# Performance work log

Measured on AMD Instinct MI355X. Metric: run time of the kernel, lower is better.

## Reference

```python
import jax, jax.numpy as jnp
import numpy as np

N_NODES = 10000
N_EDGES = 640000
NODE_DIM = 128
EDGE_DIM = 32
OUT_DIM = 128


def setup_inputs() -> dict:
    key = jax.random.key(0)
    k_h, k_e, k_ef, k_w1, k_w2 = jax.random.split(key, 5)
    h = jax.random.normal(k_h, (N_NODES, NODE_DIM), dtype=jnp.float32)
    edge_index = jax.random.randint(k_e, (2, N_EDGES), 0, N_NODES, dtype=jnp.int64)
    edge_features = jax.random.normal(k_ef, (N_EDGES, EDGE_DIM), dtype=jnp.float32)
    in_dim = 2 * NODE_DIM + EDGE_DIM
    # Kaiming-ish init scale for realism
    W1 = jax.random.normal(k_w1, (in_dim, OUT_DIM), dtype=jnp.float32) / np.sqrt(in_dim)
    b1 = jnp.zeros((OUT_DIM,), dtype=jnp.float32)
    W2 = jax.random.normal(k_w2, (OUT_DIM, OUT_DIM), dtype=jnp.float32) / np.sqrt(OUT_DIM)
    b2 = jnp.zeros((OUT_DIM,), dtype=jnp.float32)
    return {"h": h, "edge_index": edge_index, "edge_features": edge_features,
            "n": N_NODES, "W1": W1, "b1": b1, "W2": W2, "b2": b2}


def reference(h, edge_index, edge_features, n, W1, b1, W2, b2):
    rows, cols = edge_index[0], edge_index[1]
    # gather source/target node features + edge features -> [E, 2*node_dim+edge_dim]
    msg_input = jnp.concatenate([h[rows], h[cols], edge_features], axis=-1)
    hidden = jax.nn.relu(msg_input @ W1 + b1)   # [E, out_dim]
    messages = hidden @ W2 + b2                 # [E, out_dim]
    # scatter-add messages onto destination rows -> [n, out_dim]
    out = jax.ops.segment_sum(messages, rows, num_segments=n)
    return out
```

## Files before the change

### kernel.cpp

```cpp
#include <hip/hip_runtime.h>
#include <hip/hip_bf16.h>


typedef __attribute__((ext_vector_type(8))) short bf16x8;
typedef __attribute__((ext_vector_type(4))) float f32x4;

#define ND 128
#define ED 32

__device__ __forceinline__ short f2bf(float x) {
  unsigned int u = __float_as_uint(x);
  unsigned int r = (u + 0x7FFFu + ((u >> 16) & 1u)) >> 16;
  return (short)r;
}

__device__ __forceinline__ float bf2f(short s) {
  return __uint_as_float(((unsigned int)(unsigned short)s) << 16);
}

__device__ __forceinline__ f32x4 bf8lo(bf16x8 v) {
  f32x4 r;
  #pragma unroll
  for (int j = 0; j < 4; ++j) r[j] = bf2f(v[j]);
  return r;
}
__device__ __forceinline__ f32x4 bf8hi(bf16x8 v) {
  f32x4 r;
  #pragma unroll
  for (int j = 0; j < 4; ++j) r[j] = bf2f(v[4 + j]);
  return r;
}

__device__ __forceinline__ int load_idx(const void* ei, long long i, int is64) {
  return is64 ? (int)((const long long*)ei)[i] : ((const int*)ei)[i];
}

__device__ __forceinline__ int detect64(const void* ei) {
  const unsigned int* u = (const unsigned int*)ei;
  int is64 = 1;
  #pragma unroll
  for (int i = 0; i < 16; ++i)
    if (u[2 * i + 1] != 0u) is64 = 0;
  return is64;
}

__device__ __forceinline__ int swz(int c) {
  int ct = c >> 4, cc = c & 15;
  return (ct >> 2) * 64 + (cc >> 2) * 16 + (ct & 3) * 4 + (cc & 3);
}

__global__ __launch_bounds__(256) void prep_hist_kernel(
    const float* __restrict__ W1, const float* __restrict__ W2,
    const void* __restrict__ ei, int* __restrict__ counts,
    int* __restrict__ rank, short* __restrict__ w12t,
    short* __restrict__ w1eA, short* __restrict__ w2t, int E) {
  int b = blockIdx.x;
  if (b < 128) {
    int t = b * 256 + threadIdx.x;
    if (t < 256 * 128) {
      int np = t >> 7, k = t & 127;
      float v = (np < 128) ? W1[k * 128 + np] : W1[(128 + k) * 128 + (np - 128)];
      w12t[t] = f2bf(v);
    }
    if (t < 128 * 128) {
      int n = t >> 7, k = t & 127;
      w2t[t] = f2bf(W2[k * 128 + n]);
    }
    if (t < 8 * 64 * 8) {
      int ct = t >> 9, lane = (t >> 3) & 63, j = t & 7;
      int li = lane & 15, lg = lane >> 4;
      w1eA[t] = f2bf(W1[(256 + lg * 8 + j) * 128 + ct * 16 + li]);
    }
  } else {
    int e = (b - 128) * 256 + threadIdx.x;
    if (e < E) {
      int is64 = detect64(ei);
      int r = load_idx(ei, e, is64);
      rank[e] = atomicAdd(&counts[r], 1);
    }
  }
}

__global__ __launch_bounds__(1024) void scan_kernel(const int* __restrict__ counts,
                                                    int* __restrict__ row_ptr, int n) {
  __shared__ int wtot[16];
  int tid = threadIdx.x;
  int lane = tid & 63, w = tid >> 6;
  int base_i = tid * 16;
  int c[16];
  int tot = 0;
  #pragma unroll
  for (int j = 0; j < 16; ++j) {
    int i = base_i + j;
    c[j] = (i < n) ? counts[i] : 0;
    tot += c[j];
  }
  int x = tot;
  #pragma unroll
  for (int d = 1; d < 64; d <<= 1) {
    int t = __shfl_up(x, d);
    if (lane >= d) x += t;
  }
  if (lane == 63) wtot[w] = x;
  __syncthreads();
  if (w == 0) {
    int y = (lane < 16) ? wtot[lane] : 0;
    #pragma unroll
    for (int d = 1; d < 16; d <<= 1) {
      int t = __shfl_up(y, d);
      if (lane >= d) y += t;
    }
    if (lane < 16) wtot[lane] = y;
  }
  __syncthreads();
  int waveoff = (w == 0) ? 0 : wtot[w - 1];
  int run = waveoff + x - tot;
  if (tid == 0) row_ptr[0] = 0;
  #pragma unroll
  for (int j = 0; j < 16; ++j) {
    int i = base_i + j;
    if (i < n) {
      run += c[j];
      row_ptr[i + 1] = run;
    }
  }
}

__global__ __launch_bounds__(256, 4) void scatter_sg_kernel(
    const void* __restrict__ ei, const int* __restrict__ row_ptr,
    const int* __restrict__ rank, const float* __restrict__ h,
    const short* __restrict__ w12t, const float* __restrict__ b1,
    int2* __restrict__ ec, float* __restrict__ s2, short* __restrict__ g2,
    int N, int E) {
  int b = blockIdx.x;
  int SGB = (N + 63) >> 6;
  if (b < SGB) {
    int lane = threadIdx.x & 63, w = threadIdx.x >> 6;
    int li = lane & 15, lg = lane >> 4;
    int base = b * 64 + w * 16;
    int rowm = base + li;
    if (rowm >= N) rowm = N - 1;
    float breg[8];
    #pragma unroll
    for (int nt = 0; nt < 8; ++nt) breg[nt] = b1[nt * 16 + li];
    f32x4 acc[16];
    #pragma unroll
    for (int nt = 0; nt < 16; ++nt) acc[nt] = (f32x4){0.f, 0.f, 0.f, 0.f};
    #pragma unroll
    for (int kc = 0; kc < 4; ++kc) {
      f32x4 f0 = *(const f32x4*)(h + (size_t)rowm * ND + kc * 32 + lg * 8);
      f32x4 f1 = *(const f32x4*)(h + (size_t)rowm * ND + kc * 32 + lg * 8 + 4);
      bf16x8 a;
      #pragma unroll
      for (int j = 0; j < 4; ++j) { a[j] = f2bf(f0[j]); a[4 + j] = f2bf(f1[j]); }
      #pragma unroll
      for (int nt = 0; nt < 16; ++nt) {
        bf16x8 bb = *(const bf16x8*)(w12t + (nt * 16 + li) * 128 + kc * 32 + lg * 8);
        acc[nt] = __builtin_amdgcn_mfma_f32_16x16x32_bf16(a, bb, acc[nt], 0, 0, 0);
      }
    }
    #pragma unroll
    for (int nt = 0; nt < 16; ++nt)
      #pragma unroll
      for (int r = 0; r < 4; ++r) {
        int row = base + lg * 4 + r;
        if (row < N) {
          if (nt < 8) {
            s2[(size_t)row * 128 + swz(nt * 16 + li)] = acc[nt][r] + breg[nt];
          } else {
            g2[(size_t)row * 128 + swz((nt - 8) * 16 + li)] = f2bf(acc[nt][r]);
          }
        }
      }
  } else {
    int e = (b - SGB) * 256 + threadIdx.x;
    if (e < E) {
      int is64 = detect64(ei);
      int r = load_idx(ei, e, is64);
      int c = load_idx(ei, (long long)E + e, is64);
      ec[row_ptr[r] + rank[e]] = make_int2(e, c);
    }
  }
}

__global__ __launch_bounds__(128) void layer1_kernel(
    const float* __restrict__ s2, const short* __restrict__ g2,
    const float* __restrict__ ef, const int2* __restrict__ ec,
    const short* __restrict__ w1eA, const int* __restrict__ row_ptr,
    float* __restrict__ hsum) {
  int node = blockIdx.x;
  int lane = threadIdx.x & 63;
  int w = threadIdx.x >> 6;
  int li = lane & 15, lg = lane >> 4;
  int rp = row_ptr[node], rpe = row_ptr[node + 1];
  int deg = rpe - rp;
  __shared__ float red[128];

  f32x4 psum[8];
  #pragma unroll
  for (int ct = 0; ct < 8; ++ct) psum[ct] = (f32x4){0.f, 0.f, 0.f, 0.f};

  if (deg > 0) {
    bf16x8 wa[8];
    #pragma unroll
    for (int ct = 0; ct < 8; ++ct)
      wa[ct] = *(const bf16x8*)(w1eA + ((ct * 64 + lane) * 8));
    f32x4 sreg[8];
    #pragma unroll
    for (int ct = 0; ct < 8; ++ct)
      sreg[ct] = *(const f32x4*)(s2 + (size_t)node * 128 + (ct >> 2) * 64 + lg * 16 + (ct & 3) * 4);

    int ntiles = (deg + 15) >> 4;
    int last = rpe - 1;
    auto ppos = [&](int t) {
      int p = rp + t * 16 + li;
      return p > last ? last : p;
    };

    int2 iA = ec[ppos(w)];
    int2 iB = ec[ppos(w + 2)];
    f32x4 eA0 = *(const f32x4*)(ef + (size_t)iA.x * ED + lg * 8);
    f32x4 eA1 = *(const f32x4*)(ef + (size_t)iA.x * ED + lg * 8 + 4);
    const short* gpA = g2 + (size_t)iA.y * 128;
    bf16x8 gA00 = *(const bf16x8*)(gpA + lg * 16);
    bf16x8 gA01 = *(const bf16x8*)(gpA + lg * 16 + 8);
    bf16x8 gA10 = *(const bf16x8*)(gpA + 64 + lg * 16);
    bf16x8 gA11 = *(const bf16x8*)(gpA + 64 + lg * 16 + 8);

    for (int t = w; t < ntiles; t += 2) {
      int2 iC = ec[ppos(t + 4)];
      f32x4 eB0 = *(const f32x4*)(ef + (size_t)iB.x * ED + lg * 8);
      f32x4 eB1 = *(const f32x4*)(ef + (size_t)iB.x * ED + lg * 8 + 4);
      const short* gpB = g2 + (size_t)iB.y * 128;
      bf16x8 gB00 = *(const bf16x8*)(gpB + lg * 16);
      bf16x8 gB01 = *(const bf16x8*)(gpB + lg * 16 + 8);
      bf16x8 gB10 = *(const bf16x8*)(gpB + 64 + lg * 16);
      bf16x8 gB11 = *(const bf16x8*)(gpB + 64 + lg * 16 + 8);
      bf16x8 bfrag;
      #pragma unroll
      for (int j = 0; j < 4; ++j) { bfrag[j] = f2bf(eA0[j]); bfrag[4 + j] = f2bf(eA1[j]); }
      f32x4 acc[8];
      #pragma unroll
      for (int ct = 0; ct < 8; ++ct)
        acc[ct] = __builtin_amdgcn_mfma_f32_16x16x32_bf16(wa[ct], bfrag,
                                                          (f32x4){0.f, 0.f, 0.f, 0.f}, 0, 0, 0);
      if ((t * 16 + li) < deg) {
        #pragma unroll
        for (int ct = 0; ct < 8; ++ct) {
          bf16x8 gr = (ct < 4) ? ((ct & 2) ? gA01 : gA00) : ((ct & 2) ? gA11 : gA10);
          f32x4 gv = (ct & 1) ? bf8hi(gr) : bf8lo(gr);
          f32x4 v = acc[ct] + sreg[ct] + gv;
          #pragma unroll
          for (int r = 0; r < 4; ++r)
            psum[ct][r] += (v[r] > 0.f ? v[r] : 0.f);
        }
      }
      iA = iB; iB = iC;
      eA0 = eB0; eA1 = eB1;
      gA00 = gB00; gA01 = gB01; gA10 = gB10; gA11 = gB11;
    }
  }

  #pragma unroll
  for (int ct = 0; ct < 8; ++ct)
    #pragma unroll
    for (int r = 0; r < 4; ++r) {
      float v = psum[ct][r];
      v += __shfl_xor(v, 1);
      v += __shfl_xor(v, 2);
      v += __shfl_xor(v, 4);
      v += __shfl_xor(v, 8);
      psum[ct][r] = v;
    }
  if (w == 1 && li == 0) {
    #pragma unroll
    for (int ct = 0; ct < 8; ++ct)
      *(f32x4*)(red + ct * 16 + lg * 4) = psum[ct];
  }
  __syncthreads();
  if (w == 0 && li == 0) {
    #pragma unroll
    for (int ct = 0; ct < 8; ++ct) {
      f32x4 o = psum[ct] + *(const f32x4*)(red + ct * 16 + lg * 4);
      *(f32x4*)(hsum + (size_t)node * 128 + ct * 16 + lg * 4) = o;
    }
  }
}

__global__ __launch_bounds__(256) void out_kernel(const float* __restrict__ hsum,
                                                  const short* __restrict__ w2t,
                                                  const float* __restrict__ b2,
                                                  const int* __restrict__ row_ptr,
                                                  float* __restrict__ out, int N) {
  int lane = threadIdx.x & 63, w = threadIdx.x >> 6;
  int li = lane & 15, lg = lane >> 4;
  int base = blockIdx.x * 64 + w * 16;
  int rowm = base + li;
  if (rowm >= N) rowm = N - 1;
  float breg[8];
  #pragma unroll
  for (int nt = 0; nt < 8; ++nt) breg[nt] = b2[nt * 16 + li];
  f32x4 acc[8];
  #pragma unroll
  for (int nt = 0; nt < 8; ++nt) acc[nt] = (f32x4){0.f, 0.f, 0.f, 0.f};
  #pragma unroll
  for (int kc = 0; kc < 4; ++kc) {
    f32x4 f0 = *(const f32x4*)(hsum + (size_t)rowm * 128 + kc * 32 + lg * 8);
    f32x4 f1 = *(const f32x4*)(hsum + (size_t)rowm * 128 + kc * 32 + lg * 8 + 4);
    bf16x8 a;
    #pragma unroll
    for (int j = 0; j < 4; ++j) { a[j] = f2bf(f0[j]); a[4 + j] = f2bf(f1[j]); }
    #pragma unroll
    for (int nt = 0; nt < 8; ++nt) {
      bf16x8 bb = *(const bf16x8*)(w2t + (nt * 16 + li) * 128 + kc * 32 + lg * 8);
      acc[nt] = __builtin_amdgcn_mfma_f32_16x16x32_bf16(a, bb, acc[nt], 0, 0, 0);
    }
  }
  #pragma unroll
  for (int r = 0; r < 4; ++r) {
    int row = base + lg * 4 + r;
    if (row < N) {
      float dg = (float)(row_ptr[row + 1] - row_ptr[row]);
      #pragma unroll
      for (int nt = 0; nt < 8; ++nt)
        out[(size_t)row * 128 + nt * 16 + li] = acc[nt][r] + dg * breg[nt];
    }
  }
}

extern "C" void kernel_launch(void* const* d_in, const int* in_sizes, int n_in,
                              void* d_out, int out_size, void* d_ws, size_t ws_size,
                              hipStream_t stream) {
  const void*  ei = d_in[1];
  const float* ef = (const float*)d_in[2];
  const float* h  = (const float*)d_in[0];
  const float* W1 = (const float*)d_in[4];
  const float* b1 = (const float*)d_in[5];
  const float* W2 = (const float*)d_in[6];
  const float* b2 = (const float*)d_in[7];
  float* out = (float*)d_out;
  int N = in_sizes[0] / ND;
  int E = in_sizes[2] / ED;

  char* ws = (char*)d_ws;
  size_t off = 0;
  auto alloc = [&](size_t bytes) {
    size_t o = off;
    off = (off + bytes + 255) & ~(size_t)255;
    return o;
  };
  int*   counts  = (int*)(ws + alloc((size_t)N * 4));
  int*   row_ptr = (int*)(ws + alloc((size_t)(N + 1) * 4));
  int*   rank    = (int*)(ws + alloc((size_t)E * 4));
  short* w12t    = (short*)(ws + alloc(256 * 128 * 2));
  short* w1eA    = (short*)(ws + alloc(8 * 64 * 8 * 2));
  short* w2t     = (short*)(ws + alloc(128 * 128 * 2));
  float* s2      = (float*)(ws + alloc((size_t)N * 128 * 4));
  short* g2      = (short*)(ws + alloc((size_t)N * 128 * 2));
  float* hsumb   = (float*)(ws + alloc((size_t)N * 128 * 4));
  int2*  ec      = (int2*)(ws + alloc((size_t)E * 8));

  int SGB = (N + 63) >> 6;
  int SCB = (E + 255) / 256;

  hipMemsetAsync(counts, 0, (size_t)N * 4, stream);
  prep_hist_kernel<<<128 + (E + 255) / 256, 256, 0, stream>>>(
      W1, W2, ei, counts, rank, w12t, w1eA, w2t, E);
  scan_kernel<<<1, 1024, 0, stream>>>(counts, row_ptr, N);
  scatter_sg_kernel<<<SGB + SCB, 256, 0, stream>>>(
      ei, row_ptr, rank, h, w12t, b1, ec, s2, g2, N, E);
  layer1_kernel<<<N, 128, 0, stream>>>(s2, g2, ef, ec, w1eA, row_ptr, hsumb);
  out_kernel<<<(N + 63) / 64, 256, 0, stream>>>(hsumb, w2t, b2, row_ptr, out, N);
}
```

Baseline: 142.0 us.

## Balance layer1 work by edge chunks and split waves by output columns

Replaces per-node blocks in the message kernel with blocks covering fixed edge-count chunks, whose node ranges are found by binary search over row_ptr. The two waves now split output columns instead of edge tiles, which removes the shared-memory reduction and block barrier. Edge loads are batched four tiles at a time in place of the previous rolling prefetch. The int64 detection is computed once into a flag, and the histogram is split into its own kernel, adding a launch.

New measurement: 150.7 us. 1.06x slower.

```diff
diff --git a/kernel.cpp b/kernel.cpp
--- a/kernel.cpp
+++ b/kernel.cpp
@@ -7,6 +7,7 @@
 
 #define ND 128
 #define ED 32
+#define CH 64
 
 __device__ __forceinline__ short f2bf(float x) {
   unsigned int u = __float_as_uint(x);
@@ -35,50 +36,44 @@
   return is64 ? (int)((const long long*)ei)[i] : ((const int*)ei)[i];
 }
 
-__device__ __forceinline__ int detect64(const void* ei) {
-  const unsigned int* u = (const unsigned int*)ei;
-  int is64 = 1;
-  #pragma unroll
-  for (int i = 0; i < 16; ++i)
-    if (u[2 * i + 1] != 0u) is64 = 0;
-  return is64;
-}
-
 __device__ __forceinline__ int swz(int c) {
   int ct = c >> 4, cc = c & 15;
   return (ct >> 2) * 64 + (cc >> 2) * 16 + (ct & 3) * 4 + (cc & 3);
 }
 
-__global__ __launch_bounds__(256) void prep_hist_kernel(
+__global__ __launch_bounds__(256) void prep_kernel(
     const float* __restrict__ W1, const float* __restrict__ W2,
-    const void* __restrict__ ei, int* __restrict__ counts,
-    int* __restrict__ rank, short* __restrict__ w12t,
-    short* __restrict__ w1eA, short* __restrict__ w2t, int E) {
-  int b = blockIdx.x;
-  if (b < 128) {
-    int t = b * 256 + threadIdx.x;
-    if (t < 256 * 128) {
-      int np = t >> 7, k = t & 127;
-      float v = (np < 128) ? W1[k * 128 + np] : W1[(128 + k) * 128 + (np - 128)];
-      w12t[t] = f2bf(v);
-    }
-    if (t < 128 * 128) {
-      int n = t >> 7, k = t & 127;
-      w2t[t] = f2bf(W2[k * 128 + n]);
-    }
-    if (t < 8 * 64 * 8) {
-      int ct = t >> 9, lane = (t >> 3) & 63, j = t & 7;
-      int li = lane & 15, lg = lane >> 4;
-      w1eA[t] = f2bf(W1[(256 + lg * 8 + j) * 128 + ct * 16 + li]);
-    }
-  } else {
-    int e = (b - 128) * 256 + threadIdx.x;
-    if (e < E) {
-      int is64 = detect64(ei);
-      int r = load_idx(ei, e, is64);
-      rank[e] = atomicAdd(&counts[r], 1);
-    }
-  }
+    const unsigned int* __restrict__ ei, short* __restrict__ w12t,
+    short* __restrict__ w1eA, short* __restrict__ w2t, int* __restrict__ flag) {
+  if (blockIdx.x == 0 && threadIdx.x == 0) {
+    int is64 = 1;
+    for (int i = 0; i < 16; ++i)
+      if (ei[2 * i + 1] != 0u) is64 = 0;
+    flag[0] = is64;
+  }
+  int t = blockIdx.x * blockDim.x + threadIdx.x;
+  if (t < 256 * 128) {
+    int np = t >> 7, k = t & 127;
+    float v = (np < 128) ? W1[k * 128 + np] : W1[(128 + k) * 128 + (np - 128)];
+    w12t[t] = f2bf(v);
+  }
+  if (t < 128 * 128) {
+    int n = t >> 7, k = t & 127;
+    w2t[t] = f2bf(W2[k * 128 + n]);
+  }
+  if (t < 8 * 64 * 8) {
+    int ct = t >> 9, lane = (t >> 3) & 63, j = t & 7;
+    int li = lane & 15, lg = lane >> 4;
+    w1eA[t] = f2bf(W1[(256 + lg * 8 + j) * 128 + ct * 16 + li]);
+  }
+}
+
+__global__ void hist_kernel(const void* __restrict__ ei, const int* __restrict__ flag,
+                            int* __restrict__ counts, int* __restrict__ rank, int E) {
+  int e = blockIdx.x * blockDim.x + threadIdx.x;
+  if (e >= E) return;
+  int r = load_idx(ei, e, flag[0]);
+  rank[e] = atomicAdd(&counts[r], 1);
 }
 
 __global__ __launch_bounds__(1024) void scan_kernel(const int* __restrict__ counts,
@@ -127,13 +122,14 @@
 }
 
 __global__ __launch_bounds__(256, 4) void scatter_sg_kernel(
-    const void* __restrict__ ei, const int* __restrict__ row_ptr,
-    const int* __restrict__ rank, const float* __restrict__ h,
-    const short* __restrict__ w12t, const float* __restrict__ b1,
-    int2* __restrict__ ec, float* __restrict__ s2, short* __restrict__ g2,
-    int N, int E) {
+    const void* __restrict__ ei, const int* __restrict__ flag,
+    const int* __restrict__ row_ptr, const int* __restrict__ rank,
+    const float* __restrict__ h, const short* __restrict__ w12t,
+    const float* __restrict__ b1, int2* __restrict__ ec, int2* __restrict__ cb,
+    float* __restrict__ s2, short* __restrict__ g2, int N, int E, int nchunks) {
   int b = blockIdx.x;
   int SGB = (N + 63) >> 6;
+  int SCB = (E + 255) >> 8;
   if (b < SGB) {
     int lane = threadIdx.x & 63, w = threadIdx.x >> 6;
     int li = lane & 15, lg = lane >> 4;
@@ -172,13 +168,24 @@
           }
         }
       }
-  } else {
+  } else if (b < SGB + SCB) {
     int e = (b - SGB) * 256 + threadIdx.x;
     if (e < E) {
-      int is64 = detect64(ei);
-      int r = load_idx(ei, e, is64);
-      int c = load_idx(ei, (long long)E + e, is64);
+      int f = flag[0];
+      int r = load_idx(ei, e, f);
+      int c = load_idx(ei, (long long)E + e, f);
       ec[row_ptr[r] + rank[e]] = make_int2(e, c);
+    }
+  } else {
+    int k = (b - SGB - SCB) * 256 + threadIdx.x;
+    if (k < nchunks) {
+      int t0 = k * CH, t1 = t0 + CH;
+      int lo = 0, hi = N;
+      while (lo < hi) { int mid = (lo + hi) >> 1; if (row_ptr[mid] < t0) lo = mid + 1; else hi = mid; }
+      int na = lo;
+      hi = N;
+      while (lo < hi) { int mid = (lo + hi) >> 1; if (row_ptr[mid] < t1) lo = mid + 1; else hi = mid; }
+      cb[k] = make_int2(na, lo);
     }
   }
 }
@@ -187,102 +194,93 @@
     const float* __restrict__ s2, const short* __restrict__ g2,
     const float* __restrict__ ef, const int2* __restrict__ ec,
     const short* __restrict__ w1eA, const int* __restrict__ row_ptr,
-    float* __restrict__ hsum) {
-  int node = blockIdx.x;
+    const int2* __restrict__ cb, float* __restrict__ hsum) {
+  int2 bounds = cb[blockIdx.x];
+  int na = bounds.x, nb = bounds.y;
+  if (na >= nb) return;
   int lane = threadIdx.x & 63;
   int w = threadIdx.x >> 6;
   int li = lane & 15, lg = lane >> 4;
-  int rp = row_ptr[node], rpe = row_ptr[node + 1];
-  int deg = rpe - rp;
-  __shared__ float red[128];
-
-  f32x4 psum[8];
-  #pragma unroll
-  for (int ct = 0; ct < 8; ++ct) psum[ct] = (f32x4){0.f, 0.f, 0.f, 0.f};
-
-  if (deg > 0) {
-    bf16x8 wa[8];
-    #pragma unroll
-    for (int ct = 0; ct < 8; ++ct)
-      wa[ct] = *(const bf16x8*)(w1eA + ((ct * 64 + lane) * 8));
-    f32x4 sreg[8];
-    #pragma unroll
-    for (int ct = 0; ct < 8; ++ct)
-      sreg[ct] = *(const f32x4*)(s2 + (size_t)node * 128 + (ct >> 2) * 64 + lg * 16 + (ct & 3) * 4);
+
+  bf16x8 wa[4];
+  #pragma unroll
+  for (int nt = 0; nt < 4; ++nt)
+    wa[nt] = *(const bf16x8*)(w1eA + ((w * 4 + nt) * 64 + lane) * 8);
+
+  for (int n = na; n < nb; ++n) {
+    int rp = row_ptr[n], rpe = row_ptr[n + 1];
+    int deg = rpe - rp;
+    f32x4 sreg[4];
+    #pragma unroll
+    for (int nt = 0; nt < 4; ++nt)
+      sreg[nt] = *(const f32x4*)(s2 + (size_t)n * 128 + w * 64 + lg * 16 + nt * 4);
+    f32x4 psum[4];
+    #pragma unroll
+    for (int nt = 0; nt < 4; ++nt) psum[nt] = (f32x4){0.f, 0.f, 0.f, 0.f};
 
     int ntiles = (deg + 15) >> 4;
     int last = rpe - 1;
-    auto ppos = [&](int t) {
-      int p = rp + t * 16 + li;
-      return p > last ? last : p;
-    };
-
-    int2 iA = ec[ppos(w)];
-    int2 iB = ec[ppos(w + 2)];
-    f32x4 eA0 = *(const f32x4*)(ef + (size_t)iA.x * ED + lg * 8);
-    f32x4 eA1 = *(const f32x4*)(ef + (size_t)iA.x * ED + lg * 8 + 4);
-    const short* gpA = g2 + (size_t)iA.y * 128;
-    bf16x8 gA00 = *(const bf16x8*)(gpA + lg * 16);
-    bf16x8 gA01 = *(const bf16x8*)(gpA + lg * 16 + 8);
-    bf16x8 gA10 = *(const bf16x8*)(gpA + 64 + lg * 16);
-    bf16x8 gA11 = *(const bf16x8*)(gpA + 64 + lg * 16 + 8);
-
-    for (int t = w; t < ntiles; t += 2) {
-      int2 iC = ec[ppos(t + 4)];
-      f32x4 eB0 = *(const f32x4*)(ef + (size_t)iB.x * ED + lg * 8);
-      f32x4 eB1 = *(const f32x4*)(ef + (size_t)iB.x * ED + lg * 8 + 4);
-      const short* gpB = g2 + (size_t)iB.y * 128;
-      bf16x8 gB00 = *(const bf16x8*)(gpB + lg * 16);
-      bf16x8 gB01 = *(const bf16x8*)(gpB + lg * 16 + 8);
-      bf16x8 gB10 = *(const bf16x8*)(gpB + 64 + lg * 16);
-      bf16x8 gB11 = *(const bf16x8*)(gpB + 64 + lg * 16 + 8);
-      bf16x8 bfrag;
-      #pragma unroll
-      for (int j = 0; j < 4; ++j) { bfrag[j] = f2bf(eA0[j]); bfrag[4 + j] = f2bf(eA1[j]); }
-      f32x4 acc[8];
-      #pragma unroll
-      for (int ct = 0; ct < 8; ++ct)
-        acc[ct] = __builtin_amdgcn_mfma_f32_16x16x32_bf16(wa[ct], bfrag,
-                                                          (f32x4){0.f, 0.f, 0.f, 0.f}, 0, 0, 0);
-      if ((t * 16 + li) < deg) {
-        #pragma unroll
-        for (int ct = 0; ct < 8; ++ct) {
-          bf16x8 gr = (ct < 4) ? ((ct & 2) ? gA01 : gA00) : ((ct & 2) ? gA11 : gA10);
-          f32x4 gv = (ct & 1) ? bf8hi(gr) : bf8lo(gr);
-          f32x4 v = acc[ct] + sreg[ct] + gv;
+    for (int tb = 0; tb < ntiles; tb += 4) {
+      int nact = ntiles - tb;
+      if (nact > 4) nact = 4;
+      int2 ev[4];
+      #pragma unroll
+      for (int m = 0; m < 4; ++m) {
+        int p = rp + (tb + m) * 16 + li;
+        ev[m] = ec[p > last ? last : p];
+      }
+      f32x4 ea[4], eb[4];
+      #pragma unroll
+      for (int m = 0; m < 4; ++m) {
+        const float* ep = ef + (size_t)ev[m].x * ED + lg * 8;
+        ea[m] = *(const f32x4*)ep;
+        eb[m] = *(const f32x4*)(ep + 4);
+      }
+      #pragma unroll
+      for (int m = 0; m < 4; ++m) {
+        if (m < nact) {
+          const short* gp = g2 + (size_t)ev[m].y * 128 + w * 64 + lg * 16;
+          bf16x8 g0 = *(const bf16x8*)gp;
+          bf16x8 g1 = *(const bf16x8*)(gp + 8);
+          bf16x8 bfrag;
           #pragma unroll
-          for (int r = 0; r < 4; ++r)
-            psum[ct][r] += (v[r] > 0.f ? v[r] : 0.f);
+          for (int j = 0; j < 4; ++j) { bfrag[j] = f2bf(ea[m][j]); bfrag[4 + j] = f2bf(eb[m][j]); }
+          f32x4 a0 = __builtin_amdgcn_mfma_f32_16x16x32_bf16(wa[0], bfrag, (f32x4){0.f,0.f,0.f,0.f}, 0, 0, 0);
+          f32x4 a1 = __builtin_amdgcn_mfma_f32_16x16x32_bf16(wa[1], bfrag, (f32x4){0.f,0.f,0.f,0.f}, 0, 0, 0);
+          f32x4 a2 = __builtin_amdgcn_mfma_f32_16x16x32_bf16(wa[2], bfrag, (f32x4){0.f,0.f,0.f,0.f}, 0, 0, 0);
+          f32x4 a3 = __builtin_amdgcn_mfma_f32_16x16x32_bf16(wa[3], bfrag, (f32x4){0.f,0.f,0.f,0.f}, 0, 0, 0);
+          if ((tb + m) * 16 + li < deg) {
+            f32x4 v0 = a0 + sreg[0] + bf8lo(g0);
+            f32x4 v1 = a1 + sreg[1] + bf8hi(g0);
+            f32x4 v2 = a2 + sreg[2] + bf8lo(g1);
+            f32x4 v3 = a3 + sreg[3] + bf8hi(g1);
+            #pragma unroll
+            for (int r = 0; r < 4; ++r) {
+              psum[0][r] += (v0[r] > 0.f ? v0[r] : 0.f);
+              psum[1][r] += (v1[r] > 0.f ? v1[r] : 0.f);
+              psum[2][r] += (v2[r] > 0.f ? v2[r] : 0.f);
+              psum[3][r] += (v3[r] > 0.f ? v3[r] : 0.f);
+            }
+          }
         }
       }
-      iA = iB; iB = iC;
-      eA0 = eB0; eA1 = eB1;
-      gA00 = gB00; gA01 = gB01; gA10 = gB10; gA11 = gB11;
-    }
-  }
-
-  #pragma unroll
-  for (int ct = 0; ct < 8; ++ct)
-    #pragma unroll
-    for (int r = 0; r < 4; ++r) {
-      float v = psum[ct][r];
-      v += __shfl_xor(v, 1);
-      v += __shfl_xor(v, 2);
-      v += __shfl_xor(v, 4);
-      v += __shfl_xor(v, 8);
-      psum[ct][r] = v;
-    }
-  if (w == 1 && li == 0) {
-    #pragma unroll
-    for (int ct = 0; ct < 8; ++ct)
-      *(f32x4*)(red + ct * 16 + lg * 4) = psum[ct];
-  }
-  __syncthreads();
-  if (w == 0 && li == 0) {
-    #pragma unroll
-    for (int ct = 0; ct < 8; ++ct) {
-      f32x4 o = psum[ct] + *(const f32x4*)(red + ct * 16 + lg * 4);
-      *(f32x4*)(hsum + (size_t)node * 128 + ct * 16 + lg * 4) = o;
+    }
+
+    #pragma unroll
+    for (int nt = 0; nt < 4; ++nt)
+      #pragma unroll
+      for (int r = 0; r < 4; ++r) {
+        float v = psum[nt][r];
+        v += __shfl_xor(v, 1);
+        v += __shfl_xor(v, 2);
+        v += __shfl_xor(v, 4);
+        v += __shfl_xor(v, 8);
+        psum[nt][r] = v;
+      }
+    if (li == 0) {
+      #pragma unroll
+      for (int nt = 0; nt < 4; ++nt)
+        *(f32x4*)(hsum + (size_t)n * 128 + w * 64 + nt * 16 + lg * 4) = psum[nt];
     }
   }
 }
@@ -331,9 +329,9 @@
 extern "C" void kernel_launch(void* const* d_in, const int* in_sizes, int n_in,
                               void* d_out, int out_size, void* d_ws, size_t ws_size,
                               hipStream_t stream) {
+  const float* h  = (const float*)d_in[0];
   const void*  ei = d_in[1];
   const float* ef = (const float*)d_in[2];
-  const float* h  = (const float*)d_in[0];
   const float* W1 = (const float*)d_in[4];
   const float* b1 = (const float*)d_in[5];
   const float* W2 = (const float*)d_in[6];
@@ -341,6 +339,7 @@
   float* out = (float*)d_out;
   int N = in_sizes[0] / ND;
   int E = in_sizes[2] / ED;
+  int nchunks = (E + CH - 1) / CH;
 
   char* ws = (char*)d_ws;
   size_t off = 0;
@@ -349,6 +348,7 @@
     off = (off + bytes + 255) & ~(size_t)255;
     return o;
   };
+  int*   flag    = (int*)(ws + alloc(4));
   int*   counts  = (int*)(ws + alloc((size_t)N * 4));
   int*   row_ptr = (int*)(ws + alloc((size_t)(N + 1) * 4));
   int*   rank    = (int*)(ws + alloc((size_t)E * 4));
@@ -359,16 +359,18 @@
   short* g2      = (short*)(ws + alloc((size_t)N * 128 * 2));
   float* hsumb   = (float*)(ws + alloc((size_t)N * 128 * 4));
   int2*  ec      = (int2*)(ws + alloc((size_t)E * 8));
+  int2*  cbb     = (int2*)(ws + alloc((size_t)nchunks * 8));
 
   int SGB = (N + 63) >> 6;
-  int SCB = (E + 255) / 256;
+  int SCB = (E + 255) >> 8;
+  int CBB = (nchunks + 255) >> 8;
 
   hipMemsetAsync(counts, 0, (size_t)N * 4, stream);
-  prep_hist_kernel<<<128 + (E + 255) / 256, 256, 0, stream>>>(
-      W1, W2, ei, counts, rank, w12t, w1eA, w2t, E);
+  prep_kernel<<<128, 256, 0, stream>>>(W1, W2, (const unsigned int*)ei, w12t, w1eA, w2t, flag);
+  hist_kernel<<<(E + 255) / 256, 256, 0, stream>>>(ei, flag, counts, rank, E);
   scan_kernel<<<1, 1024, 0, stream>>>(counts, row_ptr, N);
-  scatter_sg_kernel<<<SGB + SCB, 256, 0, stream>>>(
-      ei, row_ptr, rank, h, w12t, b1, ec, s2, g2, N, E);
-  layer1_kernel<<<N, 128, 0, stream>>>(s2, g2, ef, ec, w1eA, row_ptr, hsumb);
+  scatter_sg_kernel<<<SGB + SCB + CBB, 256, 0, stream>>>(
+      ei, flag, row_ptr, rank, h, w12t, b1, ec, cbb, s2, g2, N, E, nchunks);
+  layer1_kernel<<<nchunks, 128, 0, stream>>>(s2, g2, ef, ec, w1eA, row_ptr, cbb, hsumb);
   out_kernel<<<(N + 63) / 64, 256, 0, stream>>>(hsumb, w2t, b2, row_ptr, out, N);
 }
```

## Replace CSR sort-based aggregation with edge-parallel atomic scatter into hidden sums

Applied to the files above, without the earlier changes.

Drops the scan and the scatter-to-CSR passes, along with the per-node segmented layer-1 kernel. A grid-stride edge kernel now computes relu(hidden) for each 16-edge tile, stages it in LDS, and atomically adds it into a zeroed fp32 hsum buffer. Row and column indices are packed into one 32-bit word with 16 bits each, and the source projection s2 is stored as bf16. This trades sorting and launch overhead for 82M fp32 atomics, which may contend heavily. The 16-bit packing also limits node count to 65536.

Result: slower. 337.6 us (+137.7%).

```diff
diff --git a/kernel.cpp b/kernel.cpp
--- a/kernel.cpp
+++ b/kernel.cpp
@@ -7,6 +7,7 @@
 
 #define ND 128
 #define ED 32
+#define LROW 132
 
 __device__ __forceinline__ short f2bf(float x) {
   unsigned int u = __float_as_uint(x);
@@ -31,19 +32,6 @@
   return r;
 }
 
-__device__ __forceinline__ int load_idx(const void* ei, long long i, int is64) {
-  return is64 ? (int)((const long long*)ei)[i] : ((const int*)ei)[i];
-}
-
-__device__ __forceinline__ int detect64(const void* ei) {
-  const unsigned int* u = (const unsigned int*)ei;
-  int is64 = 1;
-  #pragma unroll
-  for (int i = 0; i < 16; ++i)
-    if (u[2 * i + 1] != 0u) is64 = 0;
-  return is64;
-}
-
 __device__ __forceinline__ int swz(int c) {
   int ct = c >> 4, cc = c & 15;
   return (ct >> 2) * 64 + (cc >> 2) * 16 + (ct & 3) * 4 + (cc & 3);
@@ -52,7 +40,7 @@
 __global__ __launch_bounds__(256) void prep_hist_kernel(
     const float* __restrict__ W1, const float* __restrict__ W2,
     const void* __restrict__ ei, int* __restrict__ counts,
-    int* __restrict__ rank, short* __restrict__ w12t,
+    unsigned int* __restrict__ rcpk, short* __restrict__ w12t,
     short* __restrict__ w1eA, short* __restrict__ w2t, int E) {
   int b = blockIdx.x;
   if (b < 128) {
@@ -74,215 +62,134 @@
   } else {
     int e = (b - 128) * 256 + threadIdx.x;
     if (e < E) {
-      int is64 = detect64(ei);
-      int r = load_idx(ei, e, is64);
-      rank[e] = atomicAdd(&counts[r], 1);
-    }
-  }
-}
-
-__global__ __launch_bounds__(1024) void scan_kernel(const int* __restrict__ counts,
-                                                    int* __restrict__ row_ptr, int n) {
-  __shared__ int wtot[16];
-  int tid = threadIdx.x;
-  int lane = tid & 63, w = tid >> 6;
-  int base_i = tid * 16;
-  int c[16];
-  int tot = 0;
-  #pragma unroll
-  for (int j = 0; j < 16; ++j) {
-    int i = base_i + j;
-    c[j] = (i < n) ? counts[i] : 0;
-    tot += c[j];
-  }
-  int x = tot;
-  #pragma unroll
-  for (int d = 1; d < 64; d <<= 1) {
-    int t = __shfl_up(x, d);
-    if (lane >= d) x += t;
-  }
-  if (lane == 63) wtot[w] = x;
-  __syncthreads();
-  if (w == 0) {
-    int y = (lane < 16) ? wtot[lane] : 0;
-    #pragma unroll
-    for (int d = 1; d < 16; d <<= 1) {
-      int t = __shfl_up(y, d);
-      if (lane >= d) y += t;
-    }
-    if (lane < 16) wtot[lane] = y;
-  }
-  __syncthreads();
-  int waveoff = (w == 0) ? 0 : wtot[w - 1];
-  int run = waveoff + x - tot;
-  if (tid == 0) row_ptr[0] = 0;
-  #pragma unroll
-  for (int j = 0; j < 16; ++j) {
-    int i = base_i + j;
-    if (i < n) {
-      run += c[j];
-      row_ptr[i + 1] = run;
-    }
-  }
-}
-
-__global__ __launch_bounds__(256, 4) void scatter_sg_kernel(
-    const void* __restrict__ ei, const int* __restrict__ row_ptr,
-    const int* __restrict__ rank, const float* __restrict__ h,
-    const short* __restrict__ w12t, const float* __restrict__ b1,
-    int2* __restrict__ ec, float* __restrict__ s2, short* __restrict__ g2,
-    int N, int E) {
-  int b = blockIdx.x;
-  int SGB = (N + 63) >> 6;
-  if (b < SGB) {
-    int lane = threadIdx.x & 63, w = threadIdx.x >> 6;
-    int li = lane & 15, lg = lane >> 4;
-    int base = b * 64 + w * 16;
-    int rowm = base + li;
-    if (rowm >= N) rowm = N - 1;
-    float breg[8];
-    #pragma unroll
-    for (int nt = 0; nt < 8; ++nt) breg[nt] = b1[nt * 16 + li];
-    f32x4 acc[16];
-    #pragma unroll
-    for (int nt = 0; nt < 16; ++nt) acc[nt] = (f32x4){0.f, 0.f, 0.f, 0.f};
-    #pragma unroll
-    for (int kc = 0; kc < 4; ++kc) {
-      f32x4 f0 = *(const f32x4*)(h + (size_t)rowm * ND + kc * 32 + lg * 8);
-      f32x4 f1 = *(const f32x4*)(h + (size_t)rowm * ND + kc * 32 + lg * 8 + 4);
-      bf16x8 a;
-      #pragma unroll
-      for (int j = 0; j < 4; ++j) { a[j] = f2bf(f0[j]); a[4 + j] = f2bf(f1[j]); }
-      #pragma unroll
-      for (int nt = 0; nt < 16; ++nt) {
-        bf16x8 bb = *(const bf16x8*)(w12t + (nt * 16 + li) * 128 + kc * 32 + lg * 8);
-        acc[nt] = __builtin_amdgcn_mfma_f32_16x16x32_bf16(a, bb, acc[nt], 0, 0, 0);
+      const unsigned int* u = (const unsigned int*)ei;
+      int is64 = 1;
+      #pragma unroll
+      for (int i = 0; i < 16; ++i)
+        if (u[2 * i + 1] != 0u) is64 = 0;
+      int r, c;
+      if (is64) {
+        r = (int)((const long long*)ei)[e];
+        c = (int)((const long long*)ei)[(long long)E + e];
+      } else {
+        r = ((const int*)ei)[e];
+        c = ((const int*)ei)[E + e];
       }
-    }
-    #pragma unroll
-    for (int nt = 0; nt < 16; ++nt)
-      #pragma unroll
-      for (int r = 0; r < 4; ++r) {
-        int row = base + lg * 4 + r;
-        if (row < N) {
-          if (nt < 8) {
-            s2[(size_t)row * 128 + swz(nt * 16 + li)] = acc[nt][r] + breg[nt];
-          } else {
-            g2[(size_t)row * 128 + swz((nt - 8) * 16 + li)] = f2bf(acc[nt][r]);
-          }
-        }
+      atomicAdd(&counts[r], 1);
+      rcpk[e] = ((unsigned int)r << 16) | (unsigned int)c;
+    }
+  }
+}
+
+__global__ __launch_bounds__(256) void sg_kernel(const float* __restrict__ h,
+                                                 const short* __restrict__ w12t,
+                                                 const float* __restrict__ b1,
+                                                 short* __restrict__ s2b,
+                                                 short* __restrict__ g2, int N) {
+  int lane = threadIdx.x & 63, w = threadIdx.x >> 6;
+  int li = lane & 15, lg = lane >> 4;
+  int base = blockIdx.x * 64 + w * 16;
+  int rowm = base + li;
+  if (rowm >= N) rowm = N - 1;
+  float breg[8];
+  #pragma unroll
+  for (int nt = 0; nt < 8; ++nt) breg[nt] = b1[nt * 16 + li];
+  f32x4 acc[16];
+  #pragma unroll
+  for (int nt = 0; nt < 16; ++nt) acc[nt] = (f32x4){0.f, 0.f, 0.f, 0.f};
+  #pragma unroll
+  for (int kc = 0; kc < 4; ++kc) {
+    f32x4 f0 = *(const f32x4*)(h + (size_t)rowm * ND + kc * 32 + lg * 8);
+    f32x4 f1 = *(const f32x4*)(h + (size_t)rowm * ND + kc * 32 + lg * 8 + 4);
+    bf16x8 a;
+    #pragma unroll
+    for (int j = 0; j < 4; ++j) { a[j] = f2bf(f0[j]); a[4 + j] = f2bf(f1[j]); }
+    #pragma unroll
+    for (int nt = 0; nt < 16; ++nt) {
+      bf16x8 bb = *(const bf16x8*)(w12t + (nt * 16 + li) * 128 + kc * 32 + lg * 8);
+      acc[nt] = __builtin_amdgcn_mfma_f32_16x16x32_bf16(a, bb, acc[nt], 0, 0, 0);
+    }
+  }
+  #pragma unroll
+  for (int nt = 0; nt < 16; ++nt)
+    #pragma unroll
+    for (int r = 0; r < 4; ++r) {
+      int row = base + lg * 4 + r;
+      if (row < N) {
+        if (nt < 8)
+          s2b[(size_t)row * 128 + swz(nt * 16 + li)] = f2bf(acc[nt][r] + breg[nt]);
+        else
+          g2[(size_t)row * 128 + swz((nt - 8) * 16 + li)] = f2bf(acc[nt][r]);
       }
-  } else {
-    int e = (b - SGB) * 256 + threadIdx.x;
-    if (e < E) {
-      int is64 = detect64(ei);
-      int r = load_idx(ei, e, is64);
-      int c = load_idx(ei, (long long)E + e, is64);
-      ec[row_ptr[r] + rank[e]] = make_int2(e, c);
-    }
-  }
-}
-
-__global__ __launch_bounds__(128) void layer1_kernel(
-    const float* __restrict__ s2, const short* __restrict__ g2,
-    const float* __restrict__ ef, const int2* __restrict__ ec,
-    const short* __restrict__ w1eA, const int* __restrict__ row_ptr,
-    float* __restrict__ hsum) {
-  int node = blockIdx.x;
+    }
+}
+
+__global__ __launch_bounds__(256) void edge_kernel(
+    const unsigned int* __restrict__ rcpk, const float* __restrict__ ef,
+    const short* __restrict__ s2b, const short* __restrict__ g2,
+    const short* __restrict__ w1eA, float* __restrict__ hsum, int E) {
+  __shared__ float lds[4][16 * LROW];
+  int wv = threadIdx.x >> 6;
   int lane = threadIdx.x & 63;
-  int w = threadIdx.x >> 6;
   int li = lane & 15, lg = lane >> 4;
-  int rp = row_ptr[node], rpe = row_ptr[node + 1];
-  int deg = rpe - rp;
-  __shared__ float red[128];
-
-  f32x4 psum[8];
-  #pragma unroll
-  for (int ct = 0; ct < 8; ++ct) psum[ct] = (f32x4){0.f, 0.f, 0.f, 0.f};
-
-  if (deg > 0) {
-    bf16x8 wa[8];
+  float* myl = lds[wv];
+
+  bf16x8 wa[8];
+  #pragma unroll
+  for (int ct = 0; ct < 8; ++ct)
+    wa[ct] = *(const bf16x8*)(w1eA + (ct * 64 + lane) * 8);
+
+  int ntiles = (E + 15) >> 4;
+  int nwaves = gridDim.x * 4;
+  for (int t = blockIdx.x * 4 + wv; t < ntiles; t += nwaves) {
+    int e = t * 16 + li;
+    bool valid = e < E;
+    int ec = valid ? e : E - 1;
+    unsigned int rc = rcpk[ec];
+    int r = (int)(rc >> 16);
+    int c = (int)(rc & 0xffffu);
+    const float* ep = ef + (size_t)ec * ED + lg * 8;
+    f32x4 x0 = *(const f32x4*)ep;
+    f32x4 x1 = *(const f32x4*)(ep + 4);
+    const short* sp = s2b + (size_t)r * 128;
+    const short* gp = g2 + (size_t)c * 128;
+    bf16x8 sv[4], gv[4];
+    #pragma unroll
+    for (int p = 0; p < 4; ++p) {
+      int o = (p >> 1) * 64 + lg * 16 + (p & 1) * 8;
+      sv[p] = *(const bf16x8*)(sp + o);
+      gv[p] = *(const bf16x8*)(gp + o);
+    }
+    bf16x8 bfrag;
+    #pragma unroll
+    for (int j = 0; j < 4; ++j) { bfrag[j] = f2bf(x0[j]); bfrag[4 + j] = f2bf(x1[j]); }
+    f32x4 acc[8];
     #pragma unroll
     for (int ct = 0; ct < 8; ++ct)
-      wa[ct] = *(const bf16x8*)(w1eA + ((ct * 64 + lane) * 8));
-    f32x4 sreg[8];
-    #pragma unroll
-    for (int ct = 0; ct < 8; ++ct)
-      sreg[ct] = *(const f32x4*)(s2 + (size_t)node * 128 + (ct >> 2) * 64 + lg * 16 + (ct & 3) * 4);
-
-    int ntiles = (deg + 15) >> 4;
-    int last = rpe - 1;
-    auto ppos = [&](int t) {
-      int p = rp + t * 16 + li;
-      return p > last ? last : p;
-    };
-
-    int2 iA = ec[ppos(w)];
-    int2 iB = ec[ppos(w + 2)];
-    f32x4 eA0 = *(const f32x4*)(ef + (size_t)iA.x * ED + lg * 8);
-    f32x4 eA1 = *(const f32x4*)(ef + (size_t)iA.x * ED + lg * 8 + 4);
-    const short* gpA = g2 + (size_t)iA.y * 128;
-    bf16x8 gA00 = *(const bf16x8*)(gpA + lg * 16);
-    bf16x8 gA01 = *(const bf16x8*)(gpA + lg * 16 + 8);
-    bf16x8 gA10 = *(const bf16x8*)(gpA + 64 + lg * 16);
-    bf16x8 gA11 = *(const bf16x8*)(gpA + 64 + lg * 16 + 8);
-
-    for (int t = w; t < ntiles; t += 2) {
-      int2 iC = ec[ppos(t + 4)];
-      f32x4 eB0 = *(const f32x4*)(ef + (size_t)iB.x * ED + lg * 8);
-      f32x4 eB1 = *(const f32x4*)(ef + (size_t)iB.x * ED + lg * 8 + 4);
-      const short* gpB = g2 + (size_t)iB.y * 128;
-      bf16x8 gB00 = *(const bf16x8*)(gpB + lg * 16);
-      bf16x8 gB01 = *(const bf16x8*)(gpB + lg * 16 + 8);
-      bf16x8 gB10 = *(const bf16x8*)(gpB + 64 + lg * 16);
-      bf16x8 gB11 = *(const bf16x8*)(gpB + 64 + lg * 16 + 8);
-      bf16x8 bfrag;
-      #pragma unroll
-      for (int j = 0; j < 4; ++j) { bfrag[j] = f2bf(eA0[j]); bfrag[4 + j] = f2bf(eA1[j]); }
-      f32x4 acc[8];
-      #pragma unroll
-      for (int ct = 0; ct < 8; ++ct)
-        acc[ct] = __builtin_amdgcn_mfma_f32_16x16x32_bf16(wa[ct], bfrag,
-                                                          (f32x4){0.f, 0.f, 0.f, 0.f}, 0, 0, 0);
-      if ((t * 16 + li) < deg) {
-        #pragma unroll
-        for (int ct = 0; ct < 8; ++ct) {
-          bf16x8 gr = (ct < 4) ? ((ct & 2) ? gA01 : gA00) : ((ct & 2) ? gA11 : gA10);
-          f32x4 gv = (ct & 1) ? bf8hi(gr) : bf8lo(gr);
-          f32x4 v = acc[ct] + sreg[ct] + gv;
-          #pragma unroll
-          for (int r = 0; r < 4; ++r)
-            psum[ct][r] += (v[r] > 0.f ? v[r] : 0.f);
-        }
+      acc[ct] = __builtin_amdgcn_mfma_f32_16x16x32_bf16(wa[ct], bfrag,
+                                                        (f32x4){0.f, 0.f, 0.f, 0.f}, 0, 0, 0);
+    #pragma unroll
+    for (int ct = 0; ct < 8; ++ct) {
+      int p = (ct >> 2) * 2 + ((ct >> 1) & 1);
+      f32x4 sg4 = ((ct & 1) ? bf8hi(sv[p]) : bf8lo(sv[p])) +
+                  ((ct & 1) ? bf8hi(gv[p]) : bf8lo(gv[p]));
+      f32x4 v = acc[ct] + sg4;
+      #pragma unroll
+      for (int j = 0; j < 4; ++j) v[j] = v[j] > 0.f ? v[j] : 0.f;
+      if (!valid) v = (f32x4){0.f, 0.f, 0.f, 0.f};
+      *(f32x4*)(myl + li * LROW + ct * 16 + lg * 4) = v;
+    }
+    #pragma unroll
+    for (int es = 0; es < 4; ++es) {
+      int el = es * 4 + lg;
+      int rt = __shfl(r, el);
+      float* hrow = hsum + (size_t)rt * 128;
+      #pragma unroll
+      for (int p = 0; p < 8; ++p) {
+        int col = p * 16 + li;
+        float val = myl[el * LROW + col];
+        atomicAdd(hrow + col, val);
       }
-      iA = iB; iB = iC;
-      eA0 = eB0; eA1 = eB1;
-      gA00 = gB00; gA01 = gB01; gA10 = gB10; gA11 = gB11;
-    }
-  }
-
-  #pragma unroll
-  for (int ct = 0; ct < 8; ++ct)
-    #pragma unroll
-    for (int r = 0; r < 4; ++r) {
-      float v = psum[ct][r];
-      v += __shfl_xor(v, 1);
-      v += __shfl_xor(v, 2);
-      v += __shfl_xor(v, 4);
-      v += __shfl_xor(v, 8);
-      psum[ct][r] = v;
-    }
-  if (w == 1 && li == 0) {
-    #pragma unroll
-    for (int ct = 0; ct < 8; ++ct)
-      *(f32x4*)(red + ct * 16 + lg * 4) = psum[ct];
-  }
-  __syncthreads();
-  if (w == 0 && li == 0) {
-    #pragma unroll
-    for (int ct = 0; ct < 8; ++ct) {
-      f32x4 o = psum[ct] + *(const f32x4*)(red + ct * 16 + lg * 4);
-      *(f32x4*)(hsum + (size_t)node * 128 + ct * 16 + lg * 4) = o;
     }
   }
 }
@@ -290,7 +197,7 @@
 __global__ __launch_bounds__(256) void out_kernel(const float* __restrict__ hsum,
                                                   const short* __restrict__ w2t,
                                                   const float* __restrict__ b2,
-                                                  const int* __restrict__ row_ptr,
+                                                  const int* __restrict__ counts,
                                                   float* __restrict__ out, int N) {
   int lane = threadIdx.x & 63, w = threadIdx.x >> 6;
   int li = lane & 15, lg = lane >> 4;
@@ -320,7 +227,7 @@
   for (int r = 0; r < 4; ++r) {
     int row = base + lg * 4 + r;
     if (row < N) {
-      float dg = (float)(row_ptr[row + 1] - row_ptr[row]);
+      float dg = (float)counts[row];
       #pragma unroll
       for (int nt = 0; nt < 8; ++nt)
         out[(size_t)row * 128 + nt * 16 + li] = acc[nt][r] + dg * breg[nt];
@@ -331,9 +238,9 @@
 extern "C" void kernel_launch(void* const* d_in, const int* in_sizes, int n_in,
                               void* d_out, int out_size, void* d_ws, size_t ws_size,
                               hipStream_t stream) {
+  const float* h  = (const float*)d_in[0];
   const void*  ei = d_in[1];
   const float* ef = (const float*)d_in[2];
-  const float* h  = (const float*)d_in[0];
   const float* W1 = (const float*)d_in[4];
   const float* b1 = (const float*)d_in[5];
   const float* W2 = (const float*)d_in[6];
@@ -349,26 +256,20 @@
     off = (off + bytes + 255) & ~(size_t)255;
     return o;
   };
-  int*   counts  = (int*)(ws + alloc((size_t)N * 4));
-  int*   row_ptr = (int*)(ws + alloc((size_t)(N + 1) * 4));
-  int*   rank    = (int*)(ws + alloc((size_t)E * 4));
-  short* w12t    = (short*)(ws + alloc(256 * 128 * 2));
-  short* w1eA    = (short*)(ws + alloc(8 * 64 * 8 * 2));
-  short* w2t     = (short*)(ws + alloc(128 * 128 * 2));
-  float* s2      = (float*)(ws + alloc((size_t)N * 128 * 4));
-  short* g2      = (short*)(ws + alloc((size_t)N * 128 * 2));
-  float* hsumb   = (float*)(ws + alloc((size_t)N * 128 * 4));
-  int2*  ec      = (int2*)(ws + alloc((size_t)E * 8));
-
-  int SGB = (N + 63) >> 6;
-  int SCB = (E + 255) / 256;
+  int*          counts = (int*)(ws + alloc((size_t)N * 4));
+  unsigned int* rcpk   = (unsigned int*)(ws + alloc((size_t)E * 4));
+  short*        w12t   = (short*)(ws + alloc(256 * 128 * 2));
+  short*        w1eA   = (short*)(ws + alloc(8 * 64 * 8 * 2));
+  short*        w2t    = (short*)(ws + alloc(128 * 128 * 2));
+  short*        s2b    = (short*)(ws + alloc((size_t)N * 128 * 2));
+  short*        g2     = (short*)(ws + alloc((size_t)N * 128 * 2));
+  float*        hsumb  = (float*)(ws + alloc((size_t)N * 128 * 4));
 
   hipMemsetAsync(counts, 0, (size_t)N * 4, stream);
+  hipMemsetAsync(hsumb, 0, (size_t)N * 128 * 4, stream);
   prep_hist_kernel<<<128 + (E + 255) / 256, 256, 0, stream>>>(
-      W1, W2, ei, counts, rank, w12t, w1eA, w2t, E);
-  scan_kernel<<<1, 1024, 0, stream>>>(counts, row_ptr, N);
-  scatter_sg_kernel<<<SGB + SCB, 256, 0, stream>>>(
-      ei, row_ptr, rank, h, w12t, b1, ec, s2, g2, N, E);
-  layer1_kernel<<<N, 128, 0, stream>>>(s2, g2, ef, ec, w1eA, row_ptr, hsumb);
-  out_kernel<<<(N + 63) / 64, 256, 0, stream>>>(hsumb, w2t, b2, row_ptr, out, N);
-}
+      W1, W2, ei, counts, rcpk, w12t, w1eA, w2t, E);
+  sg_kernel<<<(N + 63) / 64, 256, 0, stream>>>(h, w12t, b1, s2b, g2, N);
+  edge_kernel<<<1024, 256, 0, stream>>>(rcpk, ef, s2b, g2, w1eA, hsumb, E);
+  out_kernel<<<(N + 63) / 64, 256, 0, stream>>>(hsumb, w2t, b2, counts, out, N);
+}
```
